# Optimization experiments

Hardware: AMD Instinct MI355X
Metric: run time of the kernel (lower is better)

Reference implementation:

```python
import math
import jax
import jax.numpy as jnp
import numpy as np

B = 4096        # number of contexts / segments
T = 262144      # total objects across all segments (avg 64 per segment)
F = 128         # object_size
H = 256         # hidden_size
C = 512         # context_size


def setup_inputs() -> dict:
    key = jax.random.key(0)
    ks = jax.random.split(key, 8)
    objects = jax.random.normal(ks[0], (T, F), dtype=jnp.float32)
    context = jax.random.normal(ks[1], (B, C), dtype=jnp.float32)
    # sorted segment ids; guarantee every segment non-empty by seeding one id per segment
    extra = jax.random.randint(ks[2], (T - B,), 0, B)
    segment_ids = jnp.sort(jnp.concatenate([jnp.arange(B, dtype=extra.dtype), extra])).astype(jnp.int32)
    s = 0.05
    return {
        "objects": objects,
        "context": context,
        "segment_ids": segment_ids,
        "W1": jax.random.normal(ks[3], (F, H), dtype=jnp.float32) * s,
        "b1": jnp.zeros((H,), dtype=jnp.float32),
        "W2": jax.random.normal(ks[4], (H, H), dtype=jnp.float32) * s,
        "b2": jnp.zeros((H,), dtype=jnp.float32),
        "W3": jax.random.normal(ks[5], (H, 2 * H), dtype=jnp.float32) * s,
        "b3": jnp.zeros((2 * H,), dtype=jnp.float32),
        "Wq": jax.random.normal(ks[6], (C, H), dtype=jnp.float32) * s,
        "bq": jnp.zeros((H,), dtype=jnp.float32),
    }


def reference(objects, context, segment_ids, W1, b1, W2, b2, W3, b3, Wq, bq):
    num_segments = context.shape[0]
    # kv MLP: Linear -> ReLU -> Linear -> ReLU -> Linear(2H)
    h = jax.nn.relu(objects @ W1 + b1)
    h = jax.nn.relu(h @ W2 + b2)
    kv = h @ W3 + b3                                   # [T, 2H]
    k, v = jnp.split(kv, 2, axis=1)                    # [T, H] each
    # query per object via repeat_interleave == gather by segment id
    q = (context @ Wq + bq)[segment_ids]               # [T, H]
    logits = jnp.sum(q * k, axis=1) / math.sqrt(k.shape[1])   # [T]
    # per-segment stable softmax
    m = jax.ops.segment_max(logits, segment_ids, num_segments=num_segments)
    e = jnp.exp(logits - m[segment_ids])
    z = jax.ops.segment_sum(e, segment_ids, num_segments=num_segments)
    w = e / z[segment_ids]                             # [T]
    # per-segment weighted sum of values
    embedding = jax.ops.segment_sum(w[:, None] * v, segment_ids, num_segments=num_segments)  # [B, H]
    return embedding, w
```

## Files before the change

### kernel.cpp

```cpp
#include <hip/hip_runtime.h>
#include <hip/hip_bf16.h>

#define T_TOTAL 262144
#define B_SEG   4096

typedef __attribute__((ext_vector_type(8))) short short8;
typedef __attribute__((ext_vector_type(4))) float f32x4;

__device__ __forceinline__ short f2bf(float x) {
    __hip_bfloat16 h = __float2bfloat16(x);
    return *reinterpret_cast<short*>(&h);
}
__device__ __forceinline__ float bf2f(short s) {
    unsigned u = ((unsigned)(unsigned short)s) << 16;
    return __uint_as_float(u);
}

__global__ __launch_bounds__(256) void transpose_weights(
    const float* __restrict__ W1, const float* __restrict__ W2,
    const float* __restrict__ W3,
    short* __restrict__ W1T, short* __restrict__ W2T, short* __restrict__ W3vT) {
    __shared__ float t[64][68];
    const int b = blockIdx.x, tid = threadIdx.x;
    const float* src; short* dst;
    int k0, n0_src, n0_dst, sstride, dstride;
    if (b < 8) {
        int kt = b >> 2, nt = b & 3;
        src = W1; dst = W1T; sstride = 256; dstride = 128;
        k0 = kt * 64; n0_src = nt * 64; n0_dst = nt * 64;
    } else if (b < 24) {
        int id = b - 8, kt = id >> 2, nt = id & 3;
        src = W2; dst = W2T; sstride = 256; dstride = 256;
        k0 = kt * 64; n0_src = nt * 64; n0_dst = nt * 64;
    } else {
        int id = b - 24, kt = id >> 2, nt = id & 3;
        src = W3; dst = W3vT; sstride = 512; dstride = 256;
        k0 = kt * 64; n0_src = 256 + nt * 64; n0_dst = nt * 64;
    }
    {
        int r = tid >> 4, c4 = (tid & 15) * 4;
#pragma unroll
        for (int p = 0; p < 4; p++) {
            int k = p * 16 + r;
            float4 v = *reinterpret_cast<const float4*>(&src[(size_t)(k0 + k) * sstride + n0_src + c4]);
            *reinterpret_cast<float4*>(&t[k][c4]) = v;
        }
    }
    __syncthreads();
    {
        int n = tid >> 2, kq = tid & 3;
        short8 s0, s1;
#pragma unroll
        for (int i = 0; i < 8; i++) s0[i] = f2bf(t[kq * 16 + i][n]);
#pragma unroll
        for (int i = 0; i < 8; i++) s1[i] = f2bf(t[kq * 16 + 8 + i][n]);
        short* o = &dst[(size_t)(n0_dst + n) * dstride + k0 + kq * 16];
        *reinterpret_cast<short8*>(o) = s0;
        *reinterpret_cast<short8*>(o + 8) = s1;
    }
}

__global__ __launch_bounds__(256) void vec_kernel(
    const float* __restrict__ Wq, const float* __restrict__ W3,
    const float* __restrict__ bq, const float* __restrict__ b3,
    float* __restrict__ bz, float* __restrict__ wc, float* __restrict__ c0) {
    const int tid = threadIdx.x;
    if (blockIdx.x == 0) {
        float s = 0.f;
        for (int n = 0; n < 256; n += 4) {
            float4 a = *reinterpret_cast<const float4*>(&W3[(size_t)tid * 512 + n]);
            float4 b = *reinterpret_cast<const float4*>(&bq[n]);
            s += a.x * b.x + a.y * b.y + a.z * b.z + a.w * b.w;
        }
        bz[tid] = s;
    } else {
#pragma unroll
        for (int h = 0; h < 2; h++) {
            int c = h * 256 + tid;
            float s = 0.f;
            for (int n = 0; n < 256; n += 4) {
                float4 a = *reinterpret_cast<const float4*>(&Wq[(size_t)c * 256 + n]);
                float4 b = *reinterpret_cast<const float4*>(&b3[n]);
                s += a.x * b.x + a.y * b.y + a.z * b.z + a.w * b.w;
            }
            wc[c] = s;
        }
        if (tid == 0) {
            float s = 0.f;
            for (int n = 0; n < 256; n++) s += bq[n] * b3[n];
            c0[0] = s;
        }
    }
}

__global__ __launch_bounds__(256) void prep_wqz(
    const float* __restrict__ Wq, const float* __restrict__ W3,
    float* __restrict__ Wqz) {
    __shared__ float wq[16][260];
    __shared__ float w3[16][260];
    const int tid = threadIdx.x;
    const int c0 = (blockIdx.x >> 4) * 16, j0 = (blockIdx.x & 15) * 16;
    {
        int r = tid >> 4, nq = tid & 15;
#pragma unroll
        for (int p = 0; p < 4; p++) {
            int col = nq * 4 + p * 64;
            *reinterpret_cast<float4*>(&wq[r][col]) =
                *reinterpret_cast<const float4*>(&Wq[(size_t)(c0 + r) * 256 + col]);
            *reinterpret_cast<float4*>(&w3[r][col]) =
                *reinterpret_cast<const float4*>(&W3[(size_t)(j0 + r) * 512 + col]);
        }
    }
    __syncthreads();
    const int ci = tid >> 4, ji = tid & 15;
    float s = 0.f;
    for (int n = 0; n < 256; n += 4) {
        float4 a = *reinterpret_cast<const float4*>(&wq[ci][n]);
        float4 b = *reinterpret_cast<const float4*>(&w3[ji][n]);
        s += a.x * b.x + a.y * b.y + a.z * b.z + a.w * b.w;
    }
    Wqz[(size_t)(c0 + ci) * 256 + j0 + ji] = s;
}

__global__ __launch_bounds__(256) void zq_kernel(
    const float* __restrict__ ctx, const float* __restrict__ Wqz,
    const float* __restrict__ bz, float* __restrict__ zq) {
    __shared__ float As[2][16][68];
    const int tid = threadIdx.x;
    const int tm = tid & 15, tn = tid >> 4;
    const int row0 = blockIdx.x * 64, col0 = blockIdx.y * 64;
    const int lr = tid >> 2, lk = tid & 3;

    float acc[4][4];
#pragma unroll
    for (int i = 0; i < 4; i++)
#pragma unroll
        for (int j = 0; j < 4; j++) acc[i][j] = 0.f;

    float4 av = *reinterpret_cast<const float4*>(&ctx[(size_t)(row0 + lr) * 512 + lk * 4]);
    for (int c = 0; c < 32; c++) {
        int cur = c & 1;
        As[cur][lk * 4 + 0][lr] = av.x;
        As[cur][lk * 4 + 1][lr] = av.y;
        As[cur][lk * 4 + 2][lr] = av.z;
        As[cur][lk * 4 + 3][lr] = av.w;
        __syncthreads();
        if (c < 31)
            av = *reinterpret_cast<const float4*>(
                &ctx[(size_t)(row0 + lr) * 512 + (c + 1) * 16 + lk * 4]);
#pragma unroll
        for (int k = 0; k < 16; k++) {
            float4 a = *reinterpret_cast<const float4*>(&As[cur][k][tm * 4]);
            float4 b = *reinterpret_cast<const float4*>(
                &Wqz[(size_t)(c * 16 + k) * 256 + col0 + tn * 4]);
#pragma unroll
            for (int i = 0; i < 4; i++) {
                float ai = (i == 0) ? a.x : (i == 1) ? a.y : (i == 2) ? a.z : a.w;
                acc[i][0] += ai * b.x; acc[i][1] += ai * b.y;
                acc[i][2] += ai * b.z; acc[i][3] += ai * b.w;
            }
        }
    }
    float4 bv = *reinterpret_cast<const float4*>(&bz[col0 + tn * 4]);
#pragma unroll
    for (int i = 0; i < 4; i++) {
        float4 o = {acc[i][0] + bv.x, acc[i][1] + bv.y, acc[i][2] + bv.z, acc[i][3] + bv.w};
        *reinterpret_cast<float4*>(&zq[(size_t)(row0 + tm * 4 + i) * 256 + col0 + tn * 4]) = o;
    }
}

__global__ __launch_bounds__(256) void cvec_kernel(
    const float* __restrict__ ctx, const float* __restrict__ wc,
    const float* __restrict__ c0, float* __restrict__ cbuf) {
    const int tid = threadIdx.x;
    const int row = blockIdx.x * 32 + (tid >> 3);
    const int l = tid & 7;
    float s = 0.f;
    for (int i = 0; i < 64; i += 4) {
        float4 a = *reinterpret_cast<const float4*>(&ctx[(size_t)row * 512 + l * 64 + i]);
        float4 b = *reinterpret_cast<const float4*>(&wc[l * 64 + i]);
        s += a.x * b.x + a.y * b.y + a.z * b.z + a.w * b.w;
    }
    s += __shfl_xor(s, 1); s += __shfl_xor(s, 2); s += __shfl_xor(s, 4);
    if (l == 0) cbuf[row] = s + c0[0];
}

template <int K>
__device__ __forceinline__ void run_layer(
    const short* __restrict__ act, const short* __restrict__ Wt,
    int mbase, int nbase, int l16, int quad, f32x4 acc[4][4]) {
    constexpr int KK = K / 32;
    const f32x4 zero = {0.f, 0.f, 0.f, 0.f};
#pragma unroll
    for (int i = 0; i < 4; i++)
#pragma unroll
        for (int j = 0; j < 4; j++) acc[i][j] = zero;

    short8 wreg[2][4], areg[2][4];
    int arow[4], wrow[4];
#pragma unroll
    for (int ms = 0; ms < 4; ms++) arow[ms] = mbase + ms * 16 + l16;
#pragma unroll
    for (int ns = 0; ns < 4; ns++) wrow[ns] = nbase + ns * 16 + l16;

    auto loadA = [&](int kk, int slot) {
#pragma unroll
        for (int ms = 0; ms < 4; ms++) {
            int m = arow[ms];
            int sg = (kk * 4 + quad) ^ (m & 15);
            areg[slot][ms] = *reinterpret_cast<const short8*>(&act[m * K + sg * 8]);
        }
    };
    auto loadW = [&](int kk, int slot) {
#pragma unroll
        for (int ns = 0; ns < 4; ns++)
            wreg[slot][ns] = *reinterpret_cast<const short8*>(
                &Wt[wrow[ns] * K + kk * 32 + quad * 8]);
    };

    loadW(0, 0); loadA(0, 0);
    loadW(1, 1); loadA(1, 1);
#pragma unroll
    for (int kk = 0; kk < KK; kk++) {
        int cur = kk & 1;
#pragma unroll
        for (int ms = 0; ms < 4; ms++)
#pragma unroll
            for (int ns = 0; ns < 4; ns++)
                acc[ms][ns] = __builtin_amdgcn_mfma_f32_16x16x32_bf16(
                    wreg[cur][ns], areg[cur][ms], acc[cur == cur ? ms : ms][ns], 0, 0, 0);
        if (kk + 2 < KK) { loadW(kk + 2, cur); loadA(kk + 2, cur); }
    }
}

__global__ __launch_bounds__(512, 4) void mlp_kernel(
    const float* __restrict__ objects, const int* __restrict__ seg_ids,
    const short* __restrict__ W1T, const short* __restrict__ W2T,
    const short* __restrict__ W3vT,
    const float* __restrict__ b1, const float* __restrict__ b2,
    const float* __restrict__ b3,
    const float* __restrict__ zqbuf, const float* __restrict__ cbuf,
    float* __restrict__ logits_out, short* __restrict__ vout) {
    __shared__ __align__(16) short bufH[128 * 256];
    __shared__ float slots[4][128];

    const int tid  = threadIdx.x;
    const int wave = tid >> 6;
    const int lane = tid & 63;
    const int quad = lane >> 4;
    const int l16  = lane & 15;
    const int mbase = (wave & 1) * 64;
    const int wn    = wave >> 1;
    const int nbase = wn * 64;
    const int row0  = blockIdx.x * 128;

    {
        const float4* op = reinterpret_cast<const float4*>(objects + (size_t)row0 * 128);
#pragma unroll
        for (int i = 0; i < 4; i++) {
            int u = tid + i * 512;
            int m = u >> 4, kg = u & 15;
            float4 x0 = op[u * 2];
            float4 x1 = op[u * 2 + 1];
            short8 s;
            s[0] = f2bf(x0.x); s[1] = f2bf(x0.y); s[2] = f2bf(x0.z); s[3] = f2bf(x0.w);
            s[4] = f2bf(x1.x); s[5] = f2bf(x1.y); s[6] = f2bf(x1.z); s[7] = f2bf(x1.w);
            *reinterpret_cast<short8*>(&bufH[m * 128 + ((kg ^ (m & 15)) * 8)]) = s;
        }
    }
    __syncthreads();

    f32x4 acc[4][4];

    auto store_act = [&](const float* __restrict__ bias) {
#pragma unroll
        for (int ns = 0; ns < 4; ns++) {
            int n0 = nbase + ns * 16 + quad * 4;
            float4 bv = *reinterpret_cast<const float4*>(&bias[n0]);
#pragma unroll
            for (int ms = 0; ms < 4; ms++) {
                int m = mbase + ms * 16 + l16;
                short4 s;
                s.x = f2bf(fmaxf(acc[ms][ns][0] + bv.x, 0.f));
                s.y = f2bf(fmaxf(acc[ms][ns][1] + bv.y, 0.f));
                s.z = f2bf(fmaxf(acc[ms][ns][2] + bv.z, 0.f));
                s.w = f2bf(fmaxf(acc[ms][ns][3] + bv.w, 0.f));
                *reinterpret_cast<short4*>(
                    &bufH[m * 256 + (((n0 >> 3) ^ (m & 15)) * 8) + (n0 & 7)]) = s;
            }
        }
    };

    run_layer<128>(bufH, W1T, mbase, nbase, l16, quad, acc);
    __syncthreads();
    store_act(b1);
    __syncthreads();

    run_layer<256>(bufH, W2T, mbase, nbase, l16, quad, acc);
    __syncthreads();
    {
        float part[4] = {0.f, 0.f, 0.f, 0.f};
        int segm[4];
#pragma unroll
        for (int ms = 0; ms < 4; ms++) segm[ms] = seg_ids[row0 + mbase + ms * 16 + l16];
#pragma unroll
        for (int ns = 0; ns < 4; ns++) {
            int n0 = nbase + ns * 16 + quad * 4;
            float4 bv = *reinterpret_cast<const float4*>(&b2[n0]);
#pragma unroll
            for (int ms = 0; ms < 4; ms++) {
                int m = mbase + ms * 16 + l16;
                float h0 = fmaxf(acc[ms][ns][0] + bv.x, 0.f);
                float h1v = fmaxf(acc[ms][ns][1] + bv.y, 0.f);
                float h2v = fmaxf(acc[ms][ns][2] + bv.z, 0.f);
                float h3 = fmaxf(acc[ms][ns][3] + bv.w, 0.f);
                short4 s;
                s.x = f2bf(h0); s.y = f2bf(h1v); s.z = f2bf(h2v); s.w = f2bf(h3);
                *reinterpret_cast<short4*>(
                    &bufH[m * 256 + (((n0 >> 3) ^ (m & 15)) * 8) + (n0 & 7)]) = s;
                float4 zq4 = *reinterpret_cast<const float4*>(
                    &zqbuf[(size_t)segm[ms] * 256 + n0]);
                part[ms] += h0 * zq4.x + h1v * zq4.y + h2v * zq4.z + h3 * zq4.w;
            }
        }
#pragma unroll
        for (int ms = 0; ms < 4; ms++) {
            float p = part[ms];
            p += __shfl_xor(p, 16);
            p += __shfl_xor(p, 32);
            if (quad == 0) slots[wn][mbase + ms * 16 + l16] = p;
        }
    }
    __syncthreads();
    if (tid < 128) {
        int seg = seg_ids[row0 + tid];
        float s = slots[0][tid] + slots[1][tid] + slots[2][tid] + slots[3][tid] + cbuf[seg];
        logits_out[row0 + tid] = s * 0.0625f;
    }

    run_layer<256>(bufH, W3vT, mbase, nbase, l16, quad, acc);
    __syncthreads();
#pragma unroll
    for (int ns = 0; ns < 4; ns++) {
        int n0 = nbase + ns * 16 + quad * 4;
        float4 bv = *reinterpret_cast<const float4*>(&b3[256 + n0]);
#pragma unroll
        for (int ms = 0; ms < 4; ms++) {
            int m = mbase + ms * 16 + l16;
            short4 s;
            s.x = f2bf(acc[ms][ns][0] + bv.x);
            s.y = f2bf(acc[ms][ns][1] + bv.y);
            s.z = f2bf(acc[ms][ns][2] + bv.z);
            s.w = f2bf(acc[ms][ns][3] + bv.w);
            *reinterpret_cast<short4*>(
                &bufH[m * 256 + (((n0 >> 3) ^ (m & 15)) * 8) + (n0 & 7)]) = s;
        }
    }
    __syncthreads();
#pragma unroll
    for (int i = 0; i < 8; i++) {
        int idx = tid + i * 512;
        int m = idx >> 5, sg = idx & 31;
        short8 val = *reinterpret_cast<const short8*>(&bufH[m * 256 + sg * 8]);
        int n0 = (sg ^ (m & 15)) * 8;
        *reinterpret_cast<short8*>(&vout[(size_t)(row0 + m) * 256 + n0]) = val;
    }
}

__global__ __launch_bounds__(256) void segment_kernel(
    const float* __restrict__ logits, const short* __restrict__ vbuf,
    const int* __restrict__ seg_ids, float* __restrict__ emb,
    float* __restrict__ wout) {
    const int b = blockIdx.x;
    const int tid = threadIdx.x;
    __shared__ int range[2];
    __shared__ float wred[4];
    __shared__ float slots[4][256];

    if (tid < 2) {
        int target = b + tid;
        int lo = 0, hi = T_TOTAL;
        while (lo < hi) {
            int mid = (lo + hi) >> 1;
            if (seg_ids[mid] < target) lo = mid + 1; else hi = mid;
        }
        range[tid] = lo;
    }
    __syncthreads();
    const int start = range[0], end = range[1];

    float mx = -1e30f;
    for (int t = start + tid; t < end; t += 256) mx = fmaxf(mx, logits[t]);
#pragma unroll
    for (int off = 32; off >= 1; off >>= 1) mx = fmaxf(mx, __shfl_xor(mx, off));
    if ((tid & 63) == 0) wred[tid >> 6] = mx;
    __syncthreads();
    mx = fmaxf(fmaxf(wred[0], wred[1]), fmaxf(wred[2], wred[3]));
    __syncthreads();

    float s = 0.f;
    for (int t = start + tid; t < end; t += 256) s += __expf(logits[t] - mx);
#pragma unroll
    for (int off = 32; off >= 1; off >>= 1) s += __shfl_xor(s, off);
    if ((tid & 63) == 0) wred[tid >> 6] = s;
    __syncthreads();
    float invz = 1.f / (wred[0] + wred[1] + wred[2] + wred[3]);

    for (int t = start + tid; t < end; t += 256)
        wout[t] = __expf(logits[t] - mx) * invz;

    const int cg = tid & 63, r = tid >> 6;
    float a0 = 0.f, a1 = 0.f, a2 = 0.f, a3 = 0.f;
    for (int t = start + r; t < end; t += 4) {
        float wv = __expf(logits[t] - mx) * invz;
        short4 v4 = *reinterpret_cast<const short4*>(&vbuf[(size_t)t * 256 + cg * 4]);
        a0 += wv * bf2f(v4.x);
        a1 += wv * bf2f(v4.y);
        a2 += wv * bf2f(v4.z);
        a3 += wv * bf2f(v4.w);
    }
    float4 av = {a0, a1, a2, a3};
    *reinterpret_cast<float4*>(&slots[r][cg * 4]) = av;
    __syncthreads();
    emb[(size_t)b * 256 + tid] =
        slots[0][tid] + slots[1][tid] + slots[2][tid] + slots[3][tid];
}

extern "C" void kernel_launch(void* const* d_in, const int* in_sizes, int n_in,
                              void* d_out, int out_size, void* d_ws, size_t ws_size,
                              hipStream_t stream) {
    const float* objects = (const float*)d_in[0];
    const float* context = (const float*)d_in[1];
    const int*   seg     = (const int*)d_in[2];
    const float* W1 = (const float*)d_in[3];
    const float* b1 = (const float*)d_in[4];
    const float* W2 = (const float*)d_in[5];
    const float* b2 = (const float*)d_in[6];
    const float* W3 = (const float*)d_in[7];
    const float* b3 = (const float*)d_in[8];
    const float* Wq = (const float*)d_in[9];
    const float* bq = (const float*)d_in[10];

    char* ws = (char*)d_ws;
    float* zqbuf = (float*)(ws);
    float* cbuf  = (float*)(ws + 4194304);
    short* W1T   = (short*)(ws + 4210688);
    short* W2T   = (short*)(ws + 4276224);
    short* W3vT  = (short*)(ws + 4407296);
    char*  lreg   = ws + 4538368;
    float* logits = (float*)lreg;
    float* Wqz    = (float*)lreg;
    float* bz     = (float*)(lreg + 524288);
    float* wc     = (float*)(lreg + 525312);
    float* c0     = (float*)(lreg + 527360);
    short* vbuf   = (short*)(ws + 5586944);

    float* emb  = (float*)d_out;
    float* wout = emb + (size_t)B_SEG * 256;

    transpose_weights<<<40, 256, 0, stream>>>(W1, W2, W3, W1T, W2T, W3vT);
    vec_kernel<<<2, 256, 0, stream>>>(Wq, W3, bq, b3, bz, wc, c0);
    prep_wqz<<<512, 256, 0, stream>>>(Wq, W3, Wqz);
    zq_kernel<<<dim3(64, 4), 256, 0, stream>>>(context, Wqz, bz, zqbuf);
    cvec_kernel<<<128, 256, 0, stream>>>(context, wc, c0, cbuf);
    mlp_kernel<<<T_TOTAL / 128, 512, 0, stream>>>(objects, seg, W1T, W2T, W3vT,
                                                  b1, b2, b3, zqbuf, cbuf,
                                                  logits, vbuf);
    segment_kernel<<<B_SEG, 256, 0, stream>>>(logits, vbuf, seg, emb, wout);
}
```

Before: 511.2 us.

## Fuse segment softmax into MLP and apply W3v after pooling

```diff
diff --git a/kernel.cpp b/kernel.cpp
--- a/kernel.cpp
+++ b/kernel.cpp
@@ -16,33 +16,41 @@
     return __uint_as_float(u);
 }
 
+__global__ __launch_bounds__(256) void segoff_kernel(
+    const int* __restrict__ seg_ids, int* __restrict__ seg_off) {
+    int s = blockIdx.x * 256 + threadIdx.x;
+    if (s > 4096) return;
+    if (s == 4096) { seg_off[s] = T_TOTAL; return; }
+    int lo = 0, hi = T_TOTAL;
+    while (lo < hi) {
+        int mid = (lo + hi) >> 1;
+        if (seg_ids[mid] < s) lo = mid + 1; else hi = mid;
+    }
+    seg_off[s] = lo;
+}
+
 __global__ __launch_bounds__(256) void transpose_weights(
     const float* __restrict__ W1, const float* __restrict__ W2,
-    const float* __restrict__ W3,
-    short* __restrict__ W1T, short* __restrict__ W2T, short* __restrict__ W3vT) {
+    short* __restrict__ W1T, short* __restrict__ W2T) {
     __shared__ float t[64][68];
     const int b = blockIdx.x, tid = threadIdx.x;
     const float* src; short* dst;
-    int k0, n0_src, n0_dst, sstride, dstride;
+    int k0, n0, dstride;
     if (b < 8) {
         int kt = b >> 2, nt = b & 3;
-        src = W1; dst = W1T; sstride = 256; dstride = 128;
-        k0 = kt * 64; n0_src = nt * 64; n0_dst = nt * 64;
-    } else if (b < 24) {
+        src = W1; dst = W1T; dstride = 128;
+        k0 = kt * 64; n0 = nt * 64;
+    } else {
         int id = b - 8, kt = id >> 2, nt = id & 3;
-        src = W2; dst = W2T; sstride = 256; dstride = 256;
-        k0 = kt * 64; n0_src = nt * 64; n0_dst = nt * 64;
-    } else {
-        int id = b - 24, kt = id >> 2, nt = id & 3;
-        src = W3; dst = W3vT; sstride = 512; dstride = 256;
-        k0 = kt * 64; n0_src = 256 + nt * 64; n0_dst = nt * 64;
+        src = W2; dst = W2T; dstride = 256;
+        k0 = kt * 64; n0 = nt * 64;
     }
     {
         int r = tid >> 4, c4 = (tid & 15) * 4;
 #pragma unroll
         for (int p = 0; p < 4; p++) {
             int k = p * 16 + r;
-            float4 v = *reinterpret_cast<const float4*>(&src[(size_t)(k0 + k) * sstride + n0_src + c4]);
+            float4 v = *reinterpret_cast<const float4*>(&src[(size_t)(k0 + k) * 256 + n0 + c4]);
             *reinterpret_cast<float4*>(&t[k][c4]) = v;
         }
     }
@@ -54,7 +62,7 @@
         for (int i = 0; i < 8; i++) s0[i] = f2bf(t[kq * 16 + i][n]);
 #pragma unroll
         for (int i = 0; i < 8; i++) s1[i] = f2bf(t[kq * 16 + 8 + i][n]);
-        short* o = &dst[(size_t)(n0_dst + n) * dstride + k0 + kq * 16];
+        short* o = &dst[(size_t)(n0 + n) * dstride + k0 + kq * 16];
         *reinterpret_cast<short8*>(o) = s0;
         *reinterpret_cast<short8*>(o + 8) = s1;
     }
@@ -186,244 +194,262 @@
 }
 
 template <int K>
-__device__ __forceinline__ void run_layer(
+__device__ __forceinline__ void run_layer_var(
     const short* __restrict__ act, const short* __restrict__ Wt,
-    int mbase, int nbase, int l16, int quad, f32x4 acc[4][4]) {
+    int nf, int wm, int nbase, int l16, int quad, f32x4 acc[8][4]) {
     constexpr int KK = K / 32;
     const f32x4 zero = {0.f, 0.f, 0.f, 0.f};
 #pragma unroll
-    for (int i = 0; i < 4; i++)
+    for (int i = 0; i < 8; i++)
 #pragma unroll
         for (int j = 0; j < 4; j++) acc[i][j] = zero;
 
-    short8 wreg[2][4], areg[2][4];
-    int arow[4], wrow[4];
-#pragma unroll
-    for (int ms = 0; ms < 4; ms++) arow[ms] = mbase + ms * 16 + l16;
+    short8 wreg[2][4];
+    int wrow[4];
 #pragma unroll
     for (int ns = 0; ns < 4; ns++) wrow[ns] = nbase + ns * 16 + l16;
-
-    auto loadA = [&](int kk, int slot) {
-#pragma unroll
-        for (int ms = 0; ms < 4; ms++) {
-            int m = arow[ms];
-            int sg = (kk * 4 + quad) ^ (m & 15);
-            areg[slot][ms] = *reinterpret_cast<const short8*>(&act[m * K + sg * 8]);
-        }
-    };
     auto loadW = [&](int kk, int slot) {
 #pragma unroll
         for (int ns = 0; ns < 4; ns++)
             wreg[slot][ns] = *reinterpret_cast<const short8*>(
                 &Wt[wrow[ns] * K + kk * 32 + quad * 8]);
     };
-
-    loadW(0, 0); loadA(0, 0);
-    loadW(1, 1); loadA(1, 1);
+    loadW(0, 0);
+    loadW(1, 1);
 #pragma unroll
     for (int kk = 0; kk < KK; kk++) {
+        short8 a[8];
+#pragma unroll
+        for (int i = 0; i < 8; i++) if (i < nf) {
+            int m = (wm + 2 * i) * 16 + l16;
+            int sg = (kk * 4 + quad) ^ (m & 15);
+            a[i] = *reinterpret_cast<const short8*>(&act[m * K + sg * 8]);
+        }
         int cur = kk & 1;
 #pragma unroll
-        for (int ms = 0; ms < 4; ms++)
+        for (int i = 0; i < 8; i++) if (i < nf) {
 #pragma unroll
             for (int ns = 0; ns < 4; ns++)
-                acc[ms][ns] = __builtin_amdgcn_mfma_f32_16x16x32_bf16(
-                    wreg[cur][ns], areg[cur][ms], acc[cur == cur ? ms : ms][ns], 0, 0, 0);
-        if (kk + 2 < KK) { loadW(kk + 2, cur); loadA(kk + 2, cur); }
-    }
-}
-
-__global__ __launch_bounds__(512, 4) void mlp_kernel(
+                acc[i][ns] = __builtin_amdgcn_mfma_f32_16x16x32_bf16(
+                    wreg[cur][ns], a[i], acc[i][ns], 0, 0, 0);
+        }
+        if (kk + 2 < KK) loadW(kk + 2, cur);
+    }
+}
+
+__global__ __launch_bounds__(512, 2) void fused_kernel(
     const float* __restrict__ objects, const int* __restrict__ seg_ids,
+    const int* __restrict__ seg_off,
     const short* __restrict__ W1T, const short* __restrict__ W2T,
-    const short* __restrict__ W3vT,
     const float* __restrict__ b1, const float* __restrict__ b2,
-    const float* __restrict__ b3,
     const float* __restrict__ zqbuf, const float* __restrict__ cbuf,
-    float* __restrict__ logits_out, short* __restrict__ vout) {
-    __shared__ __align__(16) short bufH[128 * 256];
-    __shared__ float slots[4][128];
+    float* __restrict__ ubuf, float* __restrict__ wout) {
+    __shared__ __align__(16) short h_lds[256 * 256];
+    __shared__ float slots[4][256];
+    __shared__ float lg[256];
+    __shared__ float tmp[256];
+    __shared__ float red[8];
+    __shared__ int sinfo[2];
 
     const int tid  = threadIdx.x;
     const int wave = tid >> 6;
     const int lane = tid & 63;
     const int quad = lane >> 4;
     const int l16  = lane & 15;
-    const int mbase = (wave & 1) * 64;
-    const int wn    = wave >> 1;
+    const int wm   = wave & 1;
+    const int wn   = wave >> 1;
     const int nbase = wn * 64;
-    const int row0  = blockIdx.x * 128;
+
+    if (tid < 2) {
+        int target = blockIdx.x * 128 + tid * 128;
+        int lo = 0, hi = 4096;
+        while (lo < hi) {
+            int mid = (lo + hi) >> 1;
+            if (seg_off[mid] < target) lo = mid + 1; else hi = mid;
+        }
+        sinfo[tid] = lo;
+    }
+    __syncthreads();
+    const int s_lo = sinfo[0], s_hi = sinfo[1];
+    if (s_lo >= s_hi) return;
+    const int r_lo = seg_off[s_lo];
+    int rows = seg_off[s_hi] - r_lo;
+    if (rows > 256) rows = 256;
+    const int mfrags = (rows + 15) >> 4;
+    const int nf = (mfrags - wm + 1) >> 1;
 
     {
-        const float4* op = reinterpret_cast<const float4*>(objects + (size_t)row0 * 128);
-#pragma unroll
-        for (int i = 0; i < 4; i++) {
-            int u = tid + i * 512;
-            int m = u >> 4, kg = u & 15;
-            float4 x0 = op[u * 2];
-            float4 x1 = op[u * 2 + 1];
+        const float* ob = objects + (size_t)r_lo * 128;
+        int cnt = rows << 4;
+        for (int i = tid; i < cnt; i += 512) {
+            int m = i >> 4, kg = i & 15;
+            const float4* p = reinterpret_cast<const float4*>(ob + m * 128 + kg * 8);
+            float4 x0 = p[0], x1 = p[1];
             short8 s;
             s[0] = f2bf(x0.x); s[1] = f2bf(x0.y); s[2] = f2bf(x0.z); s[3] = f2bf(x0.w);
             s[4] = f2bf(x1.x); s[5] = f2bf(x1.y); s[6] = f2bf(x1.z); s[7] = f2bf(x1.w);
-            *reinterpret_cast<short8*>(&bufH[m * 128 + ((kg ^ (m & 15)) * 8)]) = s;
-        }
-    }
-    __syncthreads();
-
-    f32x4 acc[4][4];
-
-    auto store_act = [&](const float* __restrict__ bias) {
-#pragma unroll
-        for (int ns = 0; ns < 4; ns++) {
-            int n0 = nbase + ns * 16 + quad * 4;
-            float4 bv = *reinterpret_cast<const float4*>(&bias[n0]);
-#pragma unroll
-            for (int ms = 0; ms < 4; ms++) {
-                int m = mbase + ms * 16 + l16;
-                short4 s;
-                s.x = f2bf(fmaxf(acc[ms][ns][0] + bv.x, 0.f));
-                s.y = f2bf(fmaxf(acc[ms][ns][1] + bv.y, 0.f));
-                s.z = f2bf(fmaxf(acc[ms][ns][2] + bv.z, 0.f));
-                s.w = f2bf(fmaxf(acc[ms][ns][3] + bv.w, 0.f));
-                *reinterpret_cast<short4*>(
-                    &bufH[m * 256 + (((n0 >> 3) ^ (m & 15)) * 8) + (n0 & 7)]) = s;
-            }
-        }
-    };
-
-    run_layer<128>(bufH, W1T, mbase, nbase, l16, quad, acc);
-    __syncthreads();
-    store_act(b1);
-    __syncthreads();
-
-    run_layer<256>(bufH, W2T, mbase, nbase, l16, quad, acc);
+            *reinterpret_cast<short8*>(&h_lds[m * 128 + ((kg ^ (m & 15)) << 3)]) = s;
+        }
+    }
+    __syncthreads();
+
+    f32x4 acc[8][4];
+
+    run_layer_var<128>(h_lds, W1T, nf, wm, nbase, l16, quad, acc);
+    __syncthreads();
+#pragma unroll
+    for (int ns = 0; ns < 4; ns++) {
+        int n0 = nbase + ns * 16 + quad * 4;
+        float4 bv = *reinterpret_cast<const float4*>(&b1[n0]);
+#pragma unroll
+        for (int i = 0; i < 8; i++) if (i < nf) {
+            int m = (wm + 2 * i) * 16 + l16;
+            short4 s;
+            s.x = f2bf(fmaxf(acc[i][ns][0] + bv.x, 0.f));
+            s.y = f2bf(fmaxf(acc[i][ns][1] + bv.y, 0.f));
+            s.z = f2bf(fmaxf(acc[i][ns][2] + bv.z, 0.f));
+            s.w = f2bf(fmaxf(acc[i][ns][3] + bv.w, 0.f));
+            *reinterpret_cast<short4*>(
+                &h_lds[m * 256 + (((n0 >> 3) ^ (m & 15)) << 3) + (n0 & 7)]) = s;
+        }
+    }
+    __syncthreads();
+
+    run_layer_var<256>(h_lds, W2T, nf, wm, nbase, l16, quad, acc);
     __syncthreads();
     {
-        float part[4] = {0.f, 0.f, 0.f, 0.f};
-        int segm[4];
-#pragma unroll
-        for (int ms = 0; ms < 4; ms++) segm[ms] = seg_ids[row0 + mbase + ms * 16 + l16];
+        float part[8];
+        int segm[8];
+#pragma unroll
+        for (int i = 0; i < 8; i++) if (i < nf) {
+            part[i] = 0.f;
+            int gr = r_lo + (wm + 2 * i) * 16 + l16;
+            segm[i] = seg_ids[gr < T_TOTAL ? gr : T_TOTAL - 1];
+        }
 #pragma unroll
         for (int ns = 0; ns < 4; ns++) {
             int n0 = nbase + ns * 16 + quad * 4;
             float4 bv = *reinterpret_cast<const float4*>(&b2[n0]);
 #pragma unroll
-            for (int ms = 0; ms < 4; ms++) {
-                int m = mbase + ms * 16 + l16;
-                float h0 = fmaxf(acc[ms][ns][0] + bv.x, 0.f);
-                float h1v = fmaxf(acc[ms][ns][1] + bv.y, 0.f);
-                float h2v = fmaxf(acc[ms][ns][2] + bv.z, 0.f);
-                float h3 = fmaxf(acc[ms][ns][3] + bv.w, 0.f);
+            for (int i = 0; i < 8; i++) if (i < nf) {
+                int m = (wm + 2 * i) * 16 + l16;
+                float h0 = fmaxf(acc[i][ns][0] + bv.x, 0.f);
+                float h1v = fmaxf(acc[i][ns][1] + bv.y, 0.f);
+                float h2v = fmaxf(acc[i][ns][2] + bv.z, 0.f);
+                float h3 = fmaxf(acc[i][ns][3] + bv.w, 0.f);
                 short4 s;
                 s.x = f2bf(h0); s.y = f2bf(h1v); s.z = f2bf(h2v); s.w = f2bf(h3);
                 *reinterpret_cast<short4*>(
-                    &bufH[m * 256 + (((n0 >> 3) ^ (m & 15)) * 8) + (n0 & 7)]) = s;
-                float4 zq4 = *reinterpret_cast<const float4*>(
-                    &zqbuf[(size_t)segm[ms] * 256 + n0]);
-                part[ms] += h0 * zq4.x + h1v * zq4.y + h2v * zq4.z + h3 * zq4.w;
+                    &h_lds[m * 256 + (((n0 >> 3) ^ (m & 15)) << 3) + (n0 & 7)]) = s;
+                float4 z = *reinterpret_cast<const float4*>(
+                    &zqbuf[(size_t)segm[i] * 256 + n0]);
+                part[i] += h0 * z.x + h1v * z.y + h2v * z.z + h3 * z.w;
             }
         }
 #pragma unroll
-        for (int ms = 0; ms < 4; ms++) {
-            float p = part[ms];
+        for (int i = 0; i < 8; i++) if (i < nf) {
+            float p = part[i];
             p += __shfl_xor(p, 16);
             p += __shfl_xor(p, 32);
-            if (quad == 0) slots[wn][mbase + ms * 16 + l16] = p;
-        }
-    }
-    __syncthreads();
-    if (tid < 128) {
-        int seg = seg_ids[row0 + tid];
-        float s = slots[0][tid] + slots[1][tid] + slots[2][tid] + slots[3][tid] + cbuf[seg];
-        logits_out[row0 + tid] = s * 0.0625f;
-    }
-
-    run_layer<256>(bufH, W3vT, mbase, nbase, l16, quad, acc);
-    __syncthreads();
-#pragma unroll
-    for (int ns = 0; ns < 4; ns++) {
-        int n0 = nbase + ns * 16 + quad * 4;
-        float4 bv = *reinterpret_cast<const float4*>(&b3[256 + n0]);
-#pragma unroll
-        for (int ms = 0; ms < 4; ms++) {
-            int m = mbase + ms * 16 + l16;
-            short4 s;
-            s.x = f2bf(acc[ms][ns][0] + bv.x);
-            s.y = f2bf(acc[ms][ns][1] + bv.y);
-            s.z = f2bf(acc[ms][ns][2] + bv.z);
-            s.w = f2bf(acc[ms][ns][3] + bv.w);
-            *reinterpret_cast<short4*>(
-                &bufH[m * 256 + (((n0 >> 3) ^ (m & 15)) * 8) + (n0 & 7)]) = s;
-        }
-    }
-    __syncthreads();
-#pragma unroll
-    for (int i = 0; i < 8; i++) {
-        int idx = tid + i * 512;
-        int m = idx >> 5, sg = idx & 31;
-        short8 val = *reinterpret_cast<const short8*>(&bufH[m * 256 + sg * 8]);
-        int n0 = (sg ^ (m & 15)) * 8;
-        *reinterpret_cast<short8*>(&vout[(size_t)(row0 + m) * 256 + n0]) = val;
-    }
-}
-
-__global__ __launch_bounds__(256) void segment_kernel(
-    const float* __restrict__ logits, const short* __restrict__ vbuf,
-    const int* __restrict__ seg_ids, float* __restrict__ emb,
-    float* __restrict__ wout) {
-    const int b = blockIdx.x;
+            if (quad == 0) slots[wn][(wm + 2 * i) * 16 + l16] = p;
+        }
+    }
+    __syncthreads();
+    if (tid < rows) {
+        int sg = seg_ids[r_lo + tid];
+        lg[tid] = (slots[0][tid] + slots[1][tid] + slots[2][tid] + slots[3][tid]
+                   + cbuf[sg]) * 0.0625f;
+    }
+    __syncthreads();
+
+    const int nn = tid & 255, half = tid >> 8;
+    for (int s = s_lo; s < s_hi; s++) {
+        int a = seg_off[s] - r_lo;
+        int e = seg_off[s + 1] - r_lo;
+        if (e > rows) e = rows;
+        int len = e - a;
+        float v = (tid < len) ? lg[a + tid] : -3.4e38f;
+#pragma unroll
+        for (int off = 32; off >= 1; off >>= 1) v = fmaxf(v, __shfl_xor(v, off));
+        if (lane == 0) red[wave] = v;
+        __syncthreads();
+        float mx = red[0];
+#pragma unroll
+        for (int i = 1; i < 8; i++) mx = fmaxf(mx, red[i]);
+        __syncthreads();
+        float ev = (tid < len) ? __expf(lg[a + tid] - mx) : 0.f;
+        float sv = ev;
+#pragma unroll
+        for (int off = 32; off >= 1; off >>= 1) sv += __shfl_xor(sv, off);
+        if (lane == 0) red[wave] = sv;
+        __syncthreads();
+        float Z = red[0] + red[1] + red[2] + red[3] + red[4] + red[5] + red[6] + red[7];
+        float invz = 1.f / Z;
+        __syncthreads();
+        if (tid < len) {
+            float w = ev * invz;
+            lg[a + tid] = w;
+            wout[r_lo + a + tid] = w;
+        }
+        __syncthreads();
+        float accu = 0.f;
+        for (int i = a + half; i < e; i += 2) {
+            int idx = i * 256 + ((((nn >> 3) ^ (i & 15)) << 3) | (nn & 7));
+            accu += lg[i] * bf2f(h_lds[idx]);
+        }
+        if (half) tmp[nn] = accu;
+        __syncthreads();
+        if (!half) ubuf[(size_t)s * 256 + nn] = accu + tmp[nn];
+        __syncthreads();
+    }
+}
+
+__global__ __launch_bounds__(256) void emb_kernel(
+    const float* __restrict__ u, const float* __restrict__ W3,
+    const float* __restrict__ b3, float* __restrict__ emb) {
+    __shared__ float As[2][16][68];
     const int tid = threadIdx.x;
-    __shared__ int range[2];
-    __shared__ float wred[4];
-    __shared__ float slots[4][256];
-
-    if (tid < 2) {
-        int target = b + tid;
-        int lo = 0, hi = T_TOTAL;
-        while (lo < hi) {
-            int mid = (lo + hi) >> 1;
-            if (seg_ids[mid] < target) lo = mid + 1; else hi = mid;
-        }
-        range[tid] = lo;
-    }
-    __syncthreads();
-    const int start = range[0], end = range[1];
-
-    float mx = -1e30f;
-    for (int t = start + tid; t < end; t += 256) mx = fmaxf(mx, logits[t]);
-#pragma unroll
-    for (int off = 32; off >= 1; off >>= 1) mx = fmaxf(mx, __shfl_xor(mx, off));
-    if ((tid & 63) == 0) wred[tid >> 6] = mx;
-    __syncthreads();
-    mx = fmaxf(fmaxf(wred[0], wred[1]), fmaxf(wred[2], wred[3]));
-    __syncthreads();
-
-    float s = 0.f;
-    for (int t = start + tid; t < end; t += 256) s += __expf(logits[t] - mx);
-#pragma unroll
-    for (int off = 32; off >= 1; off >>= 1) s += __shfl_xor(s, off);
-    if ((tid & 63) == 0) wred[tid >> 6] = s;
-    __syncthreads();
-    float invz = 1.f / (wred[0] + wred[1] + wred[2] + wred[3]);
-
-    for (int t = start + tid; t < end; t += 256)
-        wout[t] = __expf(logits[t] - mx) * invz;
-
-    const int cg = tid & 63, r = tid >> 6;
-    float a0 = 0.f, a1 = 0.f, a2 = 0.f, a3 = 0.f;
-    for (int t = start + r; t < end; t += 4) {
-        float wv = __expf(logits[t] - mx) * invz;
-        short4 v4 = *reinterpret_cast<const short4*>(&vbuf[(size_t)t * 256 + cg * 4]);
-        a0 += wv * bf2f(v4.x);
-        a1 += wv * bf2f(v4.y);
-        a2 += wv * bf2f(v4.z);
-        a3 += wv * bf2f(v4.w);
-    }
-    float4 av = {a0, a1, a2, a3};
-    *reinterpret_cast<float4*>(&slots[r][cg * 4]) = av;
-    __syncthreads();
-    emb[(size_t)b * 256 + tid] =
-        slots[0][tid] + slots[1][tid] + slots[2][tid] + slots[3][tid];
+    const int tm = tid & 15, tn = tid >> 4;
+    const int row0 = blockIdx.x * 64, col0 = blockIdx.y * 64;
+    const int lr = tid >> 2, lk = tid & 3;
+
+    float acc[4][4];
+#pragma unroll
+    for (int i = 0; i < 4; i++)
+#pragma unroll
+        for (int j = 0; j < 4; j++) acc[i][j] = 0.f;
+
+    float4 av = *reinterpret_cast<const float4*>(&u[(size_t)(row0 + lr) * 256 + lk * 4]);
+    for (int c = 0; c < 16; c++) {
+        int cur = c & 1;
+        As[cur][lk * 4 + 0][lr] = av.x;
+        As[cur][lk * 4 + 1][lr] = av.y;
+        As[cur][lk * 4 + 2][lr] = av.z;
+        As[cur][lk * 4 + 3][lr] = av.w;
+        __syncthreads();
+        if (c < 15)
+            av = *reinterpret_cast<const float4*>(
+                &u[(size_t)(row0 + lr) * 256 + (c + 1) * 16 + lk * 4]);
+#pragma unroll
+        for (int k = 0; k < 16; k++) {
+            float4 a = *reinterpret_cast<const float4*>(&As[cur][k][tm * 4]);
+            float4 b = *reinterpret_cast<const float4*>(
+                &W3[(size_t)(c * 16 + k) * 512 + 256 + col0 + tn * 4]);
+#pragma unroll
+            for (int i = 0; i < 4; i++) {
+                float ai = (i == 0) ? a.x : (i == 1) ? a.y : (i == 2) ? a.z : a.w;
+                acc[i][0] += ai * b.x; acc[i][1] += ai * b.y;
+                acc[i][2] += ai * b.z; acc[i][3] += ai * b.w;
+            }
+        }
+        __syncthreads();
+    }
+    float4 bv = *reinterpret_cast<const float4*>(&b3[256 + col0 + tn * 4]);
+#pragma unroll
+    for (int i = 0; i < 4; i++) {
+        float4 o = {acc[i][0] + bv.x, acc[i][1] + bv.y, acc[i][2] + bv.z, acc[i][3] + bv.w};
+        *reinterpret_cast<float4*>(&emb[(size_t)(row0 + tm * 4 + i) * 256 + col0 + tn * 4]) = o;
+    }
 }
 
 extern "C" void kernel_launch(void* const* d_in, const int* in_sizes, int n_in,
@@ -442,29 +468,27 @@
     const float* bq = (const float*)d_in[10];
 
     char* ws = (char*)d_ws;
-    float* zqbuf = (float*)(ws);
-    float* cbuf  = (float*)(ws + 4194304);
-    short* W1T   = (short*)(ws + 4210688);
-    short* W2T   = (short*)(ws + 4276224);
-    short* W3vT  = (short*)(ws + 4407296);
-    char*  lreg   = ws + 4538368;
-    float* logits = (float*)lreg;
-    float* Wqz    = (float*)lreg;
-    float* bz     = (float*)(lreg + 524288);
-    float* wc     = (float*)(lreg + 525312);
-    float* c0     = (float*)(lreg + 527360);
-    short* vbuf   = (short*)(ws + 5586944);
+    float* zqbuf  = (float*)(ws);
+    float* cbuf   = (float*)(ws + 4194304);
+    short* W1T    = (short*)(ws + 4210688);
+    short* W2T    = (short*)(ws + 4276224);
+    int*   seg_off= (int*)(ws + 4407296);
+    float* ubuf   = (float*)(ws + 4440064);
+    float* Wqz    = (float*)(ws + 8634368);
+    float* bz     = (float*)(ws + 9158656);
+    float* wc     = (float*)(ws + 9159680);
+    float* c0     = (float*)(ws + 9161728);
 
     float* emb  = (float*)d_out;
     float* wout = emb + (size_t)B_SEG * 256;
 
-    transpose_weights<<<40, 256, 0, stream>>>(W1, W2, W3, W1T, W2T, W3vT);
+    segoff_kernel<<<17, 256, 0, stream>>>(seg, seg_off);
+    transpose_weights<<<24, 256, 0, stream>>>(W1, W2, W1T, W2T);
     vec_kernel<<<2, 256, 0, stream>>>(Wq, W3, bq, b3, bz, wc, c0);
     prep_wqz<<<512, 256, 0, stream>>>(Wq, W3, Wqz);
     zq_kernel<<<dim3(64, 4), 256, 0, stream>>>(context, Wqz, bz, zqbuf);
     cvec_kernel<<<128, 256, 0, stream>>>(context, wc, c0, cbuf);
-    mlp_kernel<<<T_TOTAL / 128, 512, 0, stream>>>(objects, seg, W1T, W2T, W3vT,
-                                                  b1, b2, b3, zqbuf, cbuf,
-                                                  logits, vbuf);
-    segment_kernel<<<B_SEG, 256, 0, stream>>>(logits, vbuf, seg, emb, wout);
-}
+    fused_kernel<<<2048, 512, 0, stream>>>(objects, seg, seg_off, W1T, W2T,
+                                           b1, b2, zqbuf, cbuf, ubuf, wout);
+    emb_kernel<<<dim3(64, 4), 256, 0, stream>>>(ubuf, W3, b3, emb);
+}
```

Result: slower. 527.9 us (+3.3%).
